# Performance work log

Hardware: AMD Instinct MI355X
Metric: run time of the kernel (lower is better)

The kernel has to match this reference:

```python
import jax, jax.numpy as jnp
import numpy as np

B, N, D = 4, 2048, 1024
HEAD_DIMS = 128
NUM_HEADS = 8
PROJ = HEAD_DIMS * NUM_HEADS  # 1024


def setup_inputs() -> dict:
    key = jax.random.key(0)
    ks = jax.random.split(key, 5)
    # Weights stored as (in, out); xavier-normal-like scale
    def xavier(k, fan_in, fan_out):
        std = (2.0 / (fan_in + fan_out)) ** 0.5
        return jax.random.normal(k, (fan_in, fan_out), dtype=jnp.float32) * std
    return {
        "x": jax.random.normal(ks[0], (B, N, D), dtype=jnp.float32),
        "Wq": xavier(ks[1], D, PROJ),
        "Wk": xavier(ks[2], D, PROJ),
        "Wv": xavier(ks[3], D, PROJ),
        "Wo": xavier(ks[4], PROJ, PROJ),
    }


def reference(x, Wq, Wk, Wv, Wo):
    b, n, d = x.shape
    # QKV projections, split into heads: (b, h, n, hd)
    def split_heads(z):
        return z.reshape(b, n, NUM_HEADS, HEAD_DIMS).transpose(0, 2, 1, 3)
    q = split_heads(x @ Wq)
    k = split_heads(x @ Wk)
    v = split_heads(x @ Wv)
    scale = 1.0 / jnp.sqrt(jnp.float32(HEAD_DIMS))
    logits = jnp.einsum("bhqd,bhkd->bhqk", q, k) * scale
    weights = jax.nn.softmax(logits, axis=-1)
    out = jnp.einsum("bhqk,bhkd->bhqd", weights, v)
    out = out.transpose(0, 2, 1, 3).reshape(b, n, PROJ)
    return out @ Wo
```

## Files before the change

### kernel.cpp

```cpp
#include <hip/hip_runtime.h>
#include <hip/hip_bf16.h>


typedef __attribute__((ext_vector_type(8))) short short8;
typedef __attribute__((ext_vector_type(4))) short short4v;
typedef __attribute__((ext_vector_type(4))) float floatx4;

#define MFMA_BF16(a, b, c) __builtin_amdgcn_mfma_f32_16x16x32_bf16((a), (b), (c), 0, 0, 0)

static constexpr int BATCH  = 4;
static constexpr int NHEADS = 8;
static constexpr int SEQ    = 2048;
static constexpr int HD     = 128;
static constexpr int DMODEL = 1024;
static constexpr int MROWS  = BATCH * SEQ;
static constexpr int NQKV   = 3 * DMODEL;

static __device__ __forceinline__ short bf16bits(float v) {
    __hip_bfloat16 h = __float2bfloat16(v);
    return *reinterpret_cast<short*>(&h);
}

template <typename T>
static __device__ __forceinline__ short8 load8_bf16(const T* p) {
    if constexpr (sizeof(T) == 2) {
        return *(const short8*)p;
    } else {
        const float4 f0 = *(const float4*)p;
        const float4 f1 = *(const float4*)(p + 4);
        short8 r;
        r[0] = bf16bits(f0.x); r[1] = bf16bits(f0.y);
        r[2] = bf16bits(f0.z); r[3] = bf16bits(f0.w);
        r[4] = bf16bits(f1.x); r[5] = bf16bits(f1.y);
        r[6] = bf16bits(f1.z); r[7] = bf16bits(f1.w);
        return r;
    }
}

static __device__ __forceinline__ void storeC(float* C, size_t idx, float v) {
    C[idx] = v;
}
static __device__ __forceinline__ void storeC(__hip_bfloat16* C, size_t idx, float v) {
    C[idx] = __float2bfloat16(v);
}

static __device__ __forceinline__ void gload16(const short* g, short* l) {
    __builtin_amdgcn_global_load_lds(
        (const __attribute__((address_space(1))) void*)g,
        (__attribute__((address_space(3))) void*)l, 16, 0, 0);
}

__global__ __launch_bounds__(256)
void convert_bf16(const float* __restrict__ in, short* __restrict__ out)
{
    const size_t i = ((size_t)blockIdx.x * 256 + threadIdx.x) * 8;
    *(short8*)&out[i] = load8_bf16(&in[i]);
}

__global__ __launch_bounds__(256)
void transpose_w4(const float* __restrict__ W0, const float* __restrict__ W1,
                  const float* __restrict__ W2, const float* __restrict__ W3,
                  short* __restrict__ Wt, int K, int N)
{
    __shared__ short T[32][33];
    const int z = blockIdx.z;
    const float* W = (z == 0) ? W0 : (z == 1) ? W1 : (z == 2) ? W2 : W3;
    short* Wtz = Wt + (size_t)z * K * N;

    const int n0 = blockIdx.x * 32, k0 = blockIdx.y * 32;
    const int r = threadIdx.x >> 3, c4 = (threadIdx.x & 7) * 4;

    const float4 v = *(const float4*)&W[(size_t)(k0 + r) * N + n0 + c4];
    T[r][c4 + 0] = bf16bits(v.x);
    T[r][c4 + 1] = bf16bits(v.y);
    T[r][c4 + 2] = bf16bits(v.z);
    T[r][c4 + 3] = bf16bits(v.w);
    __syncthreads();

    short4v o;
    o[0] = T[c4 + 0][r]; o[1] = T[c4 + 1][r];
    o[2] = T[c4 + 2][r]; o[3] = T[c4 + 3][r];
    *(short4v*)&Wtz[(size_t)(n0 + r) * K + k0 + c4] = o;
}

__global__ __launch_bounds__(256)
void transpose_v(const short* __restrict__ V, short* __restrict__ Vt)
{
    __shared__ short T[64][72];
    const int s0 = blockIdx.x * 64;
    const int d0 = blockIdx.y * 64;
    const int bh = blockIdx.z;
    const short* Vi = V  + (size_t)bh * SEQ * HD;
    short*       Vo = Vt + (size_t)bh * HD * SEQ;

    const int r = threadIdx.x >> 3;
    const int c = threadIdx.x & 7;

    *(short8*)&T[r][c * 8]      = *(const short8*)&Vi[(size_t)(s0 + r) * HD + d0 + c * 8];
    *(short8*)&T[r + 32][c * 8] = *(const short8*)&Vi[(size_t)(s0 + r + 32) * HD + d0 + c * 8];
    __syncthreads();

    short8 o0, o1;
    #pragma unroll
    for (int j = 0; j < 8; ++j) {
        o0[j] = T[c * 8 + j][r];
        o1[j] = T[c * 8 + j][r + 32];
    }
    *(short8*)&Vo[(size_t)(d0 + r) * SEQ + s0 + c * 8]      = o0;
    *(short8*)&Vo[(size_t)(d0 + r + 32) * SEQ + s0 + c * 8] = o1;
}

template <typename OutT, bool QKV>
__global__ __launch_bounds__(256)
void gemm128(const short* __restrict__ A, const short* __restrict__ Bt,
             OutT* __restrict__ C, int M, int N, int K)
{
    __shared__ __align__(16) short As[128 * 32];
    __shared__ __align__(16) short Bs[128 * 32];

    const int tid  = threadIdx.x;
    const int lane = tid & 63;
    const int w    = tid >> 6;
    const int quad = lane >> 4;
    const int l16  = lane & 15;

    const int m0 = blockIdx.x * 128;
    const int n0 = blockIdx.y * 128;
    const int wm = (w >> 1) * 64;
    const int wn = (w & 1) * 64;

    floatx4 acc[4][4] = {};

    const int srow = w * 32 + (lane >> 2);
    const int scol = (lane & 3) * 8;
    const short* aG = A  + (size_t)(m0 + srow) * K + scol;
    const short* bG = Bt + (size_t)(n0 + srow) * K + scol;
    short* aL = As + w * 1024 + lane * 8;
    short* bL = Bs + w * 1024 + lane * 8;

    for (int k0 = 0; k0 < K; k0 += 32) {
        __syncthreads();
        gload16(aG + k0,                   aL);
        gload16(aG + k0 + (size_t)16 * K,  aL + 512);
        gload16(bG + k0,                   bL);
        gload16(bG + k0 + (size_t)16 * K,  bL + 512);
        __syncthreads();

        short8 af[4], bf[4];
        #pragma unroll
        for (int mi = 0; mi < 4; ++mi)
            af[mi] = *(short8*)&As[(wm + mi * 16 + l16) * 32 + quad * 8];
        #pragma unroll
        for (int ni = 0; ni < 4; ++ni)
            bf[ni] = *(short8*)&Bs[(wn + ni * 16 + l16) * 32 + quad * 8];

        #pragma unroll
        for (int mi = 0; mi < 4; ++mi)
            #pragma unroll
            for (int ni = 0; ni < 4; ++ni)
                acc[mi][ni] = MFMA_BF16(af[mi], bf[ni], acc[mi][ni]);
    }

    const size_t bufElems = (size_t)MROWS * DMODEL;
    #pragma unroll
    for (int mi = 0; mi < 4; ++mi)
        #pragma unroll
        for (int ni = 0; ni < 4; ++ni)
            #pragma unroll
            for (int r = 0; r < 4; ++r) {
                const int m = m0 + wm + mi * 16 + quad * 4 + r;
                const int n = n0 + wn + ni * 16 + l16;
                const float v = acc[mi][ni][r];
                if constexpr (QKV) {
                    const int qkv = n >> 10, rem = n & 1023;
                    const int h = rem >> 7, d = rem & 127;
                    const int b = m >> 11, s = m & 2047;
                    storeC(C, qkv * bufElems +
                              (((size_t)b * NHEADS + h) * SEQ + s) * HD + d, v);
                } else {
                    storeC(C, (size_t)m * N + n, v);
                }
            }
}

__global__ __launch_bounds__(512)
void attn_flash4(const short* __restrict__ Q, const short* __restrict__ K,
                 const short* __restrict__ Vt, __hip_bfloat16* __restrict__ O)
{
    __shared__ __align__(16) short Ks[64 * 128];
    __shared__ __align__(16) short Vs[128 * 64];
    __shared__ __align__(16) short Plds[8][16 * 72];

    const int tid  = threadIdx.x;
    const int lane = tid & 63;
    const int w    = tid >> 6;
    const int quad = lane >> 4;
    const int l16  = lane & 15;

    const int h  = blockIdx.x & 7;
    const int qi = blockIdx.x >> 3;
    const int b  = blockIdx.y;
    const int q0 = qi * 128;

    const short* Qh  = Q  + (((size_t)b * NHEADS + h) * SEQ) * HD;
    const short* Kh  = K  + (((size_t)b * NHEADS + h) * SEQ) * HD;
    const short* Vth = Vt + (((size_t)b * NHEADS + h) * HD) * SEQ;

    const float scale2 = 0.12752283786512624f;

    const int qrow = q0 + w * 16 + l16;
    short8 qf[4];
    #pragma unroll
    for (int c = 0; c < 4; ++c)
        qf[c] = *(const short8*)&Qh[(size_t)qrow * HD + c * 32 + quad * 8];

    const int krow = tid >> 4, kp = tid & 15;
    const short* kGA = Kh + (size_t)krow * HD + ((kp ^ (krow & 15)) * 8);
    short* kLA = Ks + tid * 8;
    const int vrow = tid >> 3, vp = tid & 7;
    const short* vGA = Vth + (size_t)vrow * SEQ + ((vp ^ (vrow & 7)) * 8);
    short* vLA = Vs + tid * 8;

    float lrow[4] = {0.f, 0.f, 0.f, 0.f};
    floatx4 acc[8] = {};

    const int swK = l16;
    const int swV = l16 & 7;
    short* Pw = &Plds[w][0];

    for (int kt = 0; kt < SEQ; kt += 64) {
        __syncthreads();
        gload16(kGA,            kLA);
        gload16(kGA + 32 * HD,  kLA + 4096);
        gload16(vGA,            vLA);
        gload16(vGA + 64 * SEQ, vLA + 4096);
        kGA += 64 * HD;
        vGA += 64;
        __syncthreads();

        floatx4 s[4] = {};
        #pragma unroll
        for (int g = 0; g < 4; ++g)
            #pragma unroll
            for (int c = 0; c < 4; ++c) {
                short8 kf = *(short8*)&Ks[(g * 16 + l16) * 128 +
                                          ((c * 4 + quad) ^ swK) * 8];
                s[g] = MFMA_BF16(qf[c], kf, s[g]);
            }

        #pragma unroll
        for (int g = 0; g < 4; ++g)
            #pragma unroll
            for (int r = 0; r < 4; ++r) {
                const float p = exp2f(fminf(s[g][r] * scale2, 28.853901f));
                lrow[r] += p;
                Pw[(quad * 4 + r) * 72 + g * 16 + l16] = bf16bits(p);
            }

        #pragma unroll
        for (int hh = 0; hh < 2; ++hh) {
            short8 pf = *(short8*)&Pw[l16 * 72 + hh * 32 + quad * 8];
            #pragma unroll
            for (int hc = 0; hc < 8; ++hc) {
                short8 vf = *(short8*)&Vs[(hc * 16 + l16) * 64 +
                                          ((hh * 4 + quad) ^ swV) * 8];
                acc[hc] = MFMA_BF16(pf, vf, acc[hc]);
            }
        }
    }

    #pragma unroll
    for (int r = 0; r < 4; ++r) {
        lrow[r] += __shfl_xor(lrow[r], 1);
        lrow[r] += __shfl_xor(lrow[r], 2);
        lrow[r] += __shfl_xor(lrow[r], 4);
        lrow[r] += __shfl_xor(lrow[r], 8);
    }

    #pragma unroll
    for (int hc = 0; hc < 8; ++hc)
        #pragma unroll
        for (int r = 0; r < 4; ++r) {
            const int row = q0 + w * 16 + quad * 4 + r;
            const float val = acc[hc][r] / fmaxf(lrow[r], 1e-30f);
            O[((size_t)b * SEQ + row) * DMODEL + h * HD + hc * 16 + l16] =
                __float2bfloat16(val);
        }
}

template <typename AT, typename OutT>
__global__ __launch_bounds__(256)
void gemm64(const AT* __restrict__ A, const float* __restrict__ W,
            OutT* __restrict__ C, int M, int N, int K, int headsplit)
{
    __shared__ __align__(16) short As[64][32];
    __shared__ __align__(16) short Bs[64][32];

    const int tid  = threadIdx.x;
    const int lane = tid & 63;
    const int w    = tid >> 6;
    const int quad = lane >> 4;
    const int l16  = lane & 15;

    const int m0 = blockIdx.x * 64;
    const int n0 = blockIdx.y * 64;
    const int wm = (w >> 1) * 32;
    const int wn = (w & 1) * 32;

    floatx4 acc[2][2] = {};

    const int arow = tid >> 2, acol = (tid & 3) * 8;
    const int brow = tid >> 3, bcol = (tid & 7) * 8;

    const AT*    aptr = A + (size_t)(m0 + arow) * K + acol;
    const float* bptr = W + (size_t)brow * N + n0 + bcol;

    for (int k0 = 0; k0 < K; k0 += 32) {
        short8 av = load8_bf16(aptr + k0);
        short8 bv = load8_bf16(bptr + (size_t)k0 * N);
        __syncthreads();
        *(short8*)&As[arow][acol] = av;
        #pragma unroll
        for (int j = 0; j < 8; ++j)
            Bs[bcol + j][brow] = bv[j];
        __syncthreads();

        short8 af0 = *(short8*)&As[wm + l16][quad * 8];
        short8 af1 = *(short8*)&As[wm + 16 + l16][quad * 8];
        short8 bf0 = *(short8*)&Bs[wn + l16][quad * 8];
        short8 bf1 = *(short8*)&Bs[wn + 16 + l16][quad * 8];

        acc[0][0] = MFMA_BF16(af0, bf0, acc[0][0]);
        acc[0][1] = MFMA_BF16(af0, bf1, acc[0][1]);
        acc[1][0] = MFMA_BF16(af1, bf0, acc[1][0]);
        acc[1][1] = MFMA_BF16(af1, bf1, acc[1][1]);
    }

    #pragma unroll
    for (int mi = 0; mi < 2; ++mi)
        #pragma unroll
        for (int ni = 0; ni < 2; ++ni)
            #pragma unroll
            for (int r = 0; r < 4; ++r) {
                const int m = m0 + wm + mi * 16 + quad * 4 + r;
                const int n = n0 + wn + ni * 16 + l16;
                const float v = acc[mi][ni][r];
                if (headsplit) {
                    const int b = m >> 11, nn = m & 2047;
                    const int h = n >> 7,  d  = n & 127;
                    storeC(C, (((size_t)b * NHEADS + h) * SEQ + nn) * HD + d, v);
                } else {
                    storeC(C, (size_t)m * N + n, v);
                }
            }
}

__global__ __launch_bounds__(256)
void attn_flash(const short* __restrict__ Q, const short* __restrict__ K,
                const short* __restrict__ V, __hip_bfloat16* __restrict__ O)
{
    __shared__ __align__(16) short Ksf[32][136];
    __shared__ __align__(16) short Vtl[HD][40];
    __shared__ __align__(16) short Pldsf[4][16][40];

    const int tid  = threadIdx.x;
    const int lane = tid & 63;
    const int w    = tid >> 6;
    const int quad = lane >> 4;
    const int l16  = lane & 15;

    const int q0 = blockIdx.x * 64;
    const int h  = blockIdx.y;
    const int b  = blockIdx.z;

    const size_t headoff = ((size_t)b * NHEADS + h) * SEQ * HD;
    const short* Qh = Q + headoff;
    const short* Kh = K + headoff;
    const short* Vh = V + headoff;

    const float scale = 0.08838834764831845f;

    const int qrow = q0 + w * 16 + l16;
    short8 qf[4];
    #pragma unroll
    for (int c = 0; c < 4; ++c)
        qf[c] = *(const short8*)&Qh[(size_t)qrow * HD + c * 32 + quad * 8];

    float mrow[4], lrow[4];
    #pragma unroll
    for (int r = 0; r < 4; ++r) { mrow[r] = -1e30f; lrow[r] = 0.f; }
    floatx4 acc[8] = {};

    const int krow = tid >> 4, kcol = (tid & 15) * 8;
    const int vkey = tid & 31;
    const int vhd  = (tid >> 5) * 16;

    for (int kt = 0; kt < SEQ; kt += 32) {
        const short* Kt = Kh + (size_t)kt * HD;
        short8 k0v = *(const short8*)(Kt + (size_t)tid * 8);
        short8 k1v = *(const short8*)(Kt + (size_t)(tid + 256) * 8);
        short8 v0 = *(const short8*)&Vh[(size_t)(kt + vkey) * HD + vhd];
        short8 v1 = *(const short8*)&Vh[(size_t)(kt + vkey) * HD + vhd + 8];

        __syncthreads();
        *(short8*)&Ksf[krow][kcol]      = k0v;
        *(short8*)&Ksf[krow + 16][kcol] = k1v;
        #pragma unroll
        for (int j = 0; j < 8; ++j) {
            Vtl[vhd + j][vkey]     = v0[j];
            Vtl[vhd + 8 + j][vkey] = v1[j];
        }
        __syncthreads();

        floatx4 s0 = {}, s1 = {};
        #pragma unroll
        for (int c = 0; c < 4; ++c) {
            short8 kf0 = *(short8*)&Ksf[l16][c * 32 + quad * 8];
            short8 kf1 = *(short8*)&Ksf[16 + l16][c * 32 + quad * 8];
            s0 = MFMA_BF16(qf[c], kf0, s0);
            s1 = MFMA_BF16(qf[c], kf1, s1);
        }

        float p0[4], p1[4], alpha[4];
        #pragma unroll
        for (int r = 0; r < 4; ++r) {
            const float a  = s0[r] * scale;
            const float bb = s1[r] * scale;
            float mx = fmaxf(a, bb);
            mx = fmaxf(mx, __shfl_xor(mx, 1));
            mx = fmaxf(mx, __shfl_xor(mx, 2));
            mx = fmaxf(mx, __shfl_xor(mx, 4));
            mx = fmaxf(mx, __shfl_xor(mx, 8));
            const float mnew = fmaxf(mrow[r], mx);
            alpha[r] = __expf(mrow[r] - mnew);
            mrow[r]  = mnew;
            p0[r] = __expf(a - mnew);
            p1[r] = __expf(bb - mnew);
            float rs = p0[r] + p1[r];
            rs += __shfl_xor(rs, 1);
            rs += __shfl_xor(rs, 2);
            rs += __shfl_xor(rs, 4);
            rs += __shfl_xor(rs, 8);
            lrow[r] = lrow[r] * alpha[r] + rs;
        }
        #pragma unroll
        for (int hc = 0; hc < 8; ++hc)
            #pragma unroll
            for (int r = 0; r < 4; ++r)
                acc[hc][r] *= alpha[r];

        #pragma unroll
        for (int r = 0; r < 4; ++r) {
            Pldsf[w][quad * 4 + r][l16]      = bf16bits(p0[r]);
            Pldsf[w][quad * 4 + r][16 + l16] = bf16bits(p1[r]);
        }
        __syncthreads();

        short8 pf = *(short8*)&Pldsf[w][l16][quad * 8];
        #pragma unroll
        for (int hc = 0; hc < 8; ++hc) {
            short8 vf = *(short8*)&Vtl[hc * 16 + l16][quad * 8];
            acc[hc] = MFMA_BF16(pf, vf, acc[hc]);
        }
    }

    #pragma unroll
    for (int hc = 0; hc < 8; ++hc)
        #pragma unroll
        for (int r = 0; r < 4; ++r) {
            const int row = q0 + w * 16 + quad * 4 + r;
            const float val = acc[hc][r] / fmaxf(lrow[r], 1e-30f);
            O[((size_t)b * SEQ + row) * DMODEL + h * HD + hc * 16 + l16] =
                __float2bfloat16(val);
        }
}

extern "C" void kernel_launch(void* const* d_in, const int* in_sizes, int n_in,
                              void* d_out, int out_size, void* d_ws, size_t ws_size,
                              hipStream_t stream)
{
    const float* x  = (const float*)d_in[0];
    const float* Wq = (const float*)d_in[1];
    const float* Wk = (const float*)d_in[2];
    const float* Wv = (const float*)d_in[3];
    const float* Wo = (const float*)d_in[4];
    float* out = (float*)d_out;

    const size_t bufElems = (size_t)MROWS * DMODEL;
    const size_t MiB = 1024 * 1024;
    dim3 tt(256);

    if (ws_size >= 72 * MiB) {
        short* xb    = (short*)d_ws;
        short* Qb    = xb + bufElems;
        short* Kb    = xb + 2 * bufElems;
        short* Vn    = xb + 3 * bufElems;
        short* Wtall = xb + 4 * bufElems;
        short* Wto   = Wtall + 3 * (size_t)DMODEL * DMODEL;
        short* VtG   = xb;
        short* Ab    = Vn;

        convert_bf16<<<dim3(MROWS * DMODEL / (256 * 8)), tt, 0, stream>>>(x, xb);

        transpose_w4<<<dim3(DMODEL / 32, DMODEL / 32, 4), tt, 0, stream>>>(
            Wq, Wk, Wv, Wo, Wtall, DMODEL, DMODEL);

        gemm128<__hip_bfloat16, true><<<dim3(MROWS / 128, NQKV / 128), tt, 0, stream>>>(
            xb, Wtall, (__hip_bfloat16*)Qb, MROWS, NQKV, DMODEL);

        transpose_v<<<dim3(SEQ / 64, HD / 64, BATCH * NHEADS), tt, 0, stream>>>(Vn, VtG);

        attn_flash4<<<dim3(NHEADS * (SEQ / 128), BATCH), dim3(512), 0, stream>>>(
            Qb, Kb, VtG, (__hip_bfloat16*)Ab);

        gemm128<float, false><<<dim3(MROWS / 128, DMODEL / 128), tt, 0, stream>>>(
            Ab, Wto, out, MROWS, DMODEL, DMODEL);
    } else {
        __hip_bfloat16* Qb = (__hip_bfloat16*)d_ws;
        __hip_bfloat16* Kb = Qb + bufElems;
        __hip_bfloat16* Vb = Kb + bufElems;
        __hip_bfloat16* Ab = Vb + bufElems;

        dim3 gg(MROWS / 64, DMODEL / 64);
        gemm64<float, __hip_bfloat16><<<gg, tt, 0, stream>>>(x, Wq, Qb, MROWS, DMODEL, DMODEL, 1);
        gemm64<float, __hip_bfloat16><<<gg, tt, 0, stream>>>(x, Wk, Kb, MROWS, DMODEL, DMODEL, 1);
        gemm64<float, __hip_bfloat16><<<gg, tt, 0, stream>>>(x, Wv, Vb, MROWS, DMODEL, DMODEL, 1);

        attn_flash<<<dim3(SEQ / 64, NHEADS, BATCH), tt, 0, stream>>>(
            (const short*)Qb, (const short*)Kb, (const short*)Vb, Ab);

        gemm64<short, float><<<gg, tt, 0, stream>>>(
            (const short*)Ab, Wo, out, MROWS, DMODEL, DMODEL, 0);
    }
}
```

Baseline: 296.3 us.

## Read V fragments directly from global memory and fold softmax scale into Q

The attention kernel no longer stages V tiles through shared memory. Each lane loads its V fragments for the PV MFMA straight from global (L2-cached) memory, which cuts shared-memory traffic and the associated staging work. Separately, the softmax scale is applied to Q in the QKV GEMM epilogue, so the per-element multiply in the attention inner loop goes away. The trade-off is that every wave now issues its own global V loads, and these are latency-exposed and duplicated across the 8 waves of a block. Rounding Q to bf16 after scaling also slightly changes numerics.

```diff
diff --git a/kernel.cpp b/kernel.cpp
--- a/kernel.cpp
+++ b/kernel.cpp
@@ -15,6 +15,8 @@
 static constexpr int DMODEL = 1024;
 static constexpr int MROWS  = BATCH * SEQ;
 static constexpr int NQKV   = 3 * DMODEL;
+
+#define QSCALE2 0.12752283786512624f
 
 static __device__ __forceinline__ short bf16bits(float v) {
     __hip_bfloat16 h = __float2bfloat16(v);
@@ -170,11 +172,12 @@
             for (int r = 0; r < 4; ++r) {
                 const int m = m0 + wm + mi * 16 + quad * 4 + r;
                 const int n = n0 + wn + ni * 16 + l16;
-                const float v = acc[mi][ni][r];
+                float v = acc[mi][ni][r];
                 if constexpr (QKV) {
                     const int qkv = n >> 10, rem = n & 1023;
                     const int h = rem >> 7, d = rem & 127;
                     const int b = m >> 11, s = m & 2047;
+                    if (qkv == 0) v *= QSCALE2;
                     storeC(C, qkv * bufElems +
                               (((size_t)b * NHEADS + h) * SEQ + s) * HD + d, v);
                 } else {
@@ -184,11 +187,10 @@
 }
 
 __global__ __launch_bounds__(512)
-void attn_flash4(const short* __restrict__ Q, const short* __restrict__ K,
+void attn_flash6(const short* __restrict__ Q, const short* __restrict__ K,
                  const short* __restrict__ Vt, __hip_bfloat16* __restrict__ O)
 {
     __shared__ __align__(16) short Ks[64 * 128];
-    __shared__ __align__(16) short Vs[128 * 64];
     __shared__ __align__(16) short Plds[8][16 * 72];
 
     const int tid  = threadIdx.x;
@@ -206,8 +208,6 @@
     const short* Kh  = K  + (((size_t)b * NHEADS + h) * SEQ) * HD;
     const short* Vth = Vt + (((size_t)b * NHEADS + h) * HD) * SEQ;
 
-    const float scale2 = 0.12752283786512624f;
-
     const int qrow = q0 + w * 16 + l16;
     short8 qf[4];
     #pragma unroll
@@ -215,27 +215,22 @@
         qf[c] = *(const short8*)&Qh[(size_t)qrow * HD + c * 32 + quad * 8];
 
     const int krow = tid >> 4, kp = tid & 15;
-    const short* kGA = Kh + (size_t)krow * HD + ((kp ^ (krow & 15)) * 8);
-    short* kLA = Ks + tid * 8;
-    const int vrow = tid >> 3, vp = tid & 7;
-    const short* vGA = Vth + (size_t)vrow * SEQ + ((vp ^ (vrow & 7)) * 8);
-    short* vLA = Vs + tid * 8;
+    const short* kG = Kh + (size_t)krow * HD + ((kp ^ (krow & 15)) * 8);
+    short* kL = Ks + tid * 8;
+
+    const short* vBase = Vth + (size_t)l16 * SEQ + quad * 8;
 
     float lrow[4] = {0.f, 0.f, 0.f, 0.f};
     floatx4 acc[8] = {};
 
     const int swK = l16;
-    const int swV = l16 & 7;
     short* Pw = &Plds[w][0];
 
     for (int kt = 0; kt < SEQ; kt += 64) {
         __syncthreads();
-        gload16(kGA,            kLA);
-        gload16(kGA + 32 * HD,  kLA + 4096);
-        gload16(vGA,            vLA);
-        gload16(vGA + 64 * SEQ, vLA + 4096);
-        kGA += 64 * HD;
-        vGA += 64;
+        gload16(kG,           kL);
+        gload16(kG + 32 * HD, kL + 4096);
+        kG += 64 * HD;
         __syncthreads();
 
         floatx4 s[4] = {};
@@ -252,7 +247,7 @@
         for (int g = 0; g < 4; ++g)
             #pragma unroll
             for (int r = 0; r < 4; ++r) {
-                const float p = exp2f(fminf(s[g][r] * scale2, 28.853901f));
+                const float p = exp2f(fminf(s[g][r], 28.853901f));
                 lrow[r] += p;
                 Pw[(quad * 4 + r) * 72 + g * 16 + l16] = bf16bits(p);
             }
@@ -262,8 +257,8 @@
             short8 pf = *(short8*)&Pw[l16 * 72 + hh * 32 + quad * 8];
             #pragma unroll
             for (int hc = 0; hc < 8; ++hc) {
-                short8 vf = *(short8*)&Vs[(hc * 16 + l16) * 64 +
-                                          ((hh * 4 + quad) ^ swV) * 8];
+                short8 vf = *(const short8*)(vBase + (size_t)(hc * 16) * SEQ +
+                                             kt + hh * 32);
                 acc[hc] = MFMA_BF16(pf, vf, acc[hc]);
             }
         }
@@ -510,7 +505,7 @@
 
         transpose_v<<<dim3(SEQ / 64, HD / 64, BATCH * NHEADS), tt, 0, stream>>>(Vn, VtG);
 
-        attn_flash4<<<dim3(NHEADS * (SEQ / 128), BATCH), dim3(512), 0, stream>>>(
+        attn_flash6<<<dim3(NHEADS * (SEQ / 128), BATCH), dim3(512), 0, stream>>>(
             Qb, Kb, VtG, (__hip_bfloat16*)Ab);
 
         gemm128<float, false><<<dim3(MROWS / 128, DMODEL / 128), tt, 0, stream>>>(
```

Result: slower. 470.1 us (+58.7%).
